# Optimization experiments

Measured on AMD Instinct MI355X. Metric: run time of the kernel, lower is better.

Reference implementation:

```python
import jax, jax.numpy as jnp
import numpy as np

N_NODES = 100000
N_EDGES = 1600000
IN_DIM, H1, H2, OUT_DIM = 128, 64, 32, 16


def setup_inputs() -> dict:
    key = jax.random.key(0)
    ks = jax.random.split(key, 9)
    x = jax.random.normal(ks[0], (N_NODES, IN_DIM), dtype=jnp.float32)
    edge_index = jax.random.randint(ks[1], (2, N_EDGES), 0, N_NODES, dtype=jnp.int64)
    # nn.Linear-style params (out_feats, in_feats) + bias
    def lin(k, o, i):
        bound = 1.0 / np.sqrt(i)
        kw, kb = jax.random.split(k)
        W = jax.random.uniform(kw, (o, i), jnp.float32, -bound, bound)
        b = jax.random.uniform(kb, (o,), jnp.float32, -bound, bound)
        return W, b
    W1, b1 = lin(ks[2], H1, IN_DIM)
    W2, b2 = lin(ks[3], H2, H1)
    Wf, bf = lin(ks[4], OUT_DIM, H2)
    return {"x": x, "edge_index": edge_index, "W1": W1, "b1": b1,
            "W2": W2, "b2": b2, "Wf": Wf, "bf": bf}


def reference(x, edge_index, W1, b1, W2, b2, Wf, bf):
    # Original: adj = to_dense_adj(edge_index); graph built from adj.T; DGL
    # copy_src+sum then gives new_h[src] = sum over dst of h[dst], i.e. A @ h
    # with A[src, dst]. No activation between layers (unused in forward),
    # dropout inactive at inference.
    N = x.shape[0]
    src, dst = edge_index[0], edge_index[1]

    def aggregate(h):  # sum of out-neighbor features: [N, d]
        return jax.ops.segment_sum(h[dst], src, num_segments=N)

    h = aggregate(x) @ W1.T + b1          # [N, 64]
    h = aggregate(h) @ W2.T + b2          # [N, 32]
    pooled = jnp.max(h, axis=0)           # [32] global max pool over nodes
    return pooled @ Wf.T + bf             # [16]
```

## Files before the change

### kernel.cpp

```cpp
#include <hip/hip_runtime.h>

#define N_NODES 100000
#define N_EDGES 1600000
#define IN_DIM 128
#define H1_DIM 64
#define H2_DIM 32
#define OUT_DIM 16

#define NPB 64
#define KB 1563
#define OFFW (KB + 1)
#define NCH 256
#define CH_E (N_EDGES / NCH)
#define CAP2 1536
#define NBIN1 64
#define NBIN2 (NCH - NBIN1)
#define NGB 782

typedef __attribute__((ext_vector_type(8))) short short8;
typedef __attribute__((ext_vector_type(4))) float f32x4;

__device__ inline unsigned short f2b(float v) {
    unsigned u = __float_as_uint(v);
    u += 0x7FFF + ((u >> 16) & 1);
    return (unsigned short)(u >> 16);
}
__device__ inline short f2bs(float v) { return (short)f2b(v); }
__device__ inline unsigned f32_to_key(float v) {
    unsigned u = __float_as_uint(v);
    return (v >= 0.f) ? (u | 0x80000000u) : ~u;
}
__device__ __forceinline__ void acc8(float* a, uint4 v) {
    a[0] += __uint_as_float(v.x << 16);
    a[1] += __uint_as_float(v.x & 0xFFFF0000u);
    a[2] += __uint_as_float(v.y << 16);
    a[3] += __uint_as_float(v.y & 0xFFFF0000u);
    a[4] += __uint_as_float(v.z << 16);
    a[5] += __uint_as_float(v.z & 0xFFFF0000u);
    a[6] += __uint_as_float(v.w << 16);
    a[7] += __uint_as_float(v.w & 0xFFFF0000u);
}

__device__ __forceinline__ void bin_chunk(const int* __restrict__ src,
                                          const int* __restrict__ dst,
                                          unsigned* __restrict__ off,
                                          unsigned* __restrict__ grec, int c) {
    __shared__ int hist[2048];
    __shared__ int part[512];
    __shared__ int cur[2048];
    int t = threadIdx.x;
    int e0 = c * CH_E;
    for (int i = t; i < 2048; i += 512) hist[i] = 0;
    __syncthreads();
    for (int e = t; e < CH_E; e += 512) atomicAdd(&hist[src[e0 + e] >> 6], 1);
    __syncthreads();
    int h0 = hist[4 * t], h1 = hist[4 * t + 1], h2 = hist[4 * t + 2], h3 = hist[4 * t + 3];
    int tot = h0 + h1 + h2 + h3;
    part[t] = tot;
    __syncthreads();
    for (int o = 1; o < 512; o <<= 1) {
        int a = (t >= o) ? part[t - o] : 0;
        __syncthreads();
        part[t] += a;
        __syncthreads();
    }
    int gb = part[t] - tot;
    int o0 = gb, o1 = gb + h0, o2 = o1 + h1, o3 = o2 + h2;
    int b4 = 4 * t;
    cur[b4] = o0; cur[b4 + 1] = o1; cur[b4 + 2] = o2; cur[b4 + 3] = o3;
    if (b4 + 0 < KB) off[(size_t)c * OFFW + b4 + 0] = o0;
    if (b4 + 1 < KB) off[(size_t)c * OFFW + b4 + 1] = o1;
    if (b4 + 2 < KB) off[(size_t)c * OFFW + b4 + 2] = o2;
    if (b4 + 3 < KB) off[(size_t)c * OFFW + b4 + 3] = o3;
    if (t == 0) off[(size_t)c * OFFW + KB] = CH_E;
    __syncthreads();
    for (int e = t; e < CH_E; e += 512) {
        int s = src[e0 + e];
        int d = dst[e0 + e];
        int p = atomicAdd(&cur[s >> 6], 1);
        grec[(size_t)e0 + p] = ((unsigned)(s & 63) << 17) | (unsigned)d;
    }
}

__global__ __launch_bounds__(512) void k1_kernel(const int* __restrict__ src,
                                                 const int* __restrict__ dst,
                                                 unsigned* __restrict__ off,
                                                 unsigned* __restrict__ grec,
                                                 const float* __restrict__ W1,
                                                 const float* __restrict__ b1,
                                                 const float* __restrict__ W2,
                                                 unsigned short* __restrict__ Wcb,
                                                 float* __restrict__ cvb) {
    if (blockIdx.x < NBIN1) {
        bin_chunk(src, dst, off, grec, blockIdx.x);
        return;
    }
    int t = threadIdx.x;
    for (int idx = t; idx < H2_DIM * IN_DIM; idx += 512) {
        int j = idx >> 7, f = idx & 127;
        float acc = 0.f;
        for (int k = 0; k < H1_DIM; ++k)
            acc += W2[j * H1_DIM + k] * W1[k * IN_DIM + f];
        Wcb[idx] = f2b(acc);
    }
    if (t < H2_DIM) {
        float s = 0.f;
        for (int k = 0; k < H1_DIM; ++k) s += W2[t * H1_DIM + k] * b1[k];
        cvb[t] = s;
    }
}

__global__ __launch_bounds__(512) void k2_kernel(const int* __restrict__ src,
                                                 const int* __restrict__ dst,
                                                 unsigned* __restrict__ off,
                                                 unsigned* __restrict__ grec,
                                                 const float* __restrict__ x,
                                                 const unsigned short* __restrict__ Wcb,
                                                 unsigned short* __restrict__ yb) {
    if (blockIdx.x < NBIN2) {
        bin_chunk(src, dst, off, grec, NBIN1 + blockIdx.x);
        return;
    }
    int gb = blockIdx.x - NBIN2;
    int t = threadIdx.x;
    int w = t >> 6, l = t & 63;
    int row = l & 15, kg = l >> 4;
    int base = gb * 128 + w * 16;
    int node = base + row;
    int nclamp = (node < N_NODES) ? node : (N_NODES - 1);
    const float* xp = x + (size_t)nclamp * IN_DIM + kg * 8;
    const unsigned short* b0p = Wcb + (size_t)row * IN_DIM + kg * 8;
    const unsigned short* b1p = Wcb + (size_t)(16 + row) * IN_DIM + kg * 8;
    f32x4 acc0 = {0.f, 0.f, 0.f, 0.f}, acc1 = {0.f, 0.f, 0.f, 0.f};
#pragma unroll
    for (int kk = 0; kk < 4; ++kk) {
        float4 xa = *(const float4*)(xp + kk * 32);
        float4 xb = *(const float4*)(xp + kk * 32 + 4);
        short8 a;
        a[0] = f2bs(xa.x); a[1] = f2bs(xa.y); a[2] = f2bs(xa.z); a[3] = f2bs(xa.w);
        a[4] = f2bs(xb.x); a[5] = f2bs(xb.y); a[6] = f2bs(xb.z); a[7] = f2bs(xb.w);
        short8 b0 = *(const short8*)(b0p + kk * 32);
        short8 b1 = *(const short8*)(b1p + kk * 32);
        acc0 = __builtin_amdgcn_mfma_f32_16x16x32_bf16(a, b0, acc0, 0, 0, 0);
        acc1 = __builtin_amdgcn_mfma_f32_16x16x32_bf16(a, b1, acc1, 0, 0, 0);
    }
#pragma unroll
    for (int r = 0; r < 4; ++r) {
        int n2 = base + kg * 4 + r;
        if (n2 < N_NODES) {
            yb[(size_t)n2 * H2_DIM + row]      = f2b(acc0[r]);
            yb[(size_t)n2 * H2_DIM + 16 + row] = f2b(acc1[r]);
        }
    }
}

__global__ __launch_bounds__(512) void agg1_kernel(const unsigned short* __restrict__ in,
                                                   const unsigned* __restrict__ off,
                                                   const unsigned* __restrict__ grec,
                                                   unsigned* __restrict__ grec2,
                                                   unsigned* __restrict__ noff,
                                                   unsigned short* __restrict__ z1b) {
    __shared__ int pos[NCH + 1], sst[NCH], len[NCH];
    __shared__ int shist[64], scur2[64];
    __shared__ int sscan[65];
    __shared__ unsigned rbuf[CAP2];
    __shared__ unsigned sbuf[CAP2];
    __shared__ int s_cnt;
    int t = threadIdx.x;
    int b = blockIdx.x;
    int gid = t >> 4;
    int L = t & 15;
    int chunk = L & 3, subset = L >> 2;

    if (t < NCH) {
        unsigned o0 = off[(size_t)t * OFFW + b];
        unsigned o1 = off[(size_t)t * OFFW + b + 1];
        sst[t] = (int)o0;
        len[t] = (int)(o1 - o0);
        pos[t] = (int)(o1 - o0);
    }
    __syncthreads();
    for (int o = 1; o < NCH; o <<= 1) {
        int a = (t < NCH && t >= o) ? pos[t - o] : 0;
        __syncthreads();
        if (t < NCH) pos[t] += a;
        __syncthreads();
    }
    if (t < NCH) pos[t] -= len[t];
    if (t == NCH - 1) {
        pos[NCH] = pos[t] + len[t];
        s_cnt = min(pos[t] + len[t], CAP2);
    }
    __syncthreads();
    int cnt = s_cnt;
    for (int i = t; i < cnt; i += 512) {
        int lo = 0, hi = NCH;
#pragma unroll
        for (int s = 0; s < 8; ++s) {
            int mid = (lo + hi) >> 1;
            if (pos[mid] <= i) lo = mid; else hi = mid;
        }
        rbuf[i] = grec[(size_t)lo * CH_E + sst[lo] + (i - pos[lo])];
    }
    if (t < 64) shist[t] = 0;
    __syncthreads();
    for (int i = t; i < cnt; i += 512) atomicAdd(&shist[rbuf[i] >> 17], 1);
    __syncthreads();
    if (t < 64) scur2[t] = shist[t];
    __syncthreads();
    for (int o = 1; o < 64; o <<= 1) {
        int a = (t < 64 && t >= o) ? scur2[t - o] : 0;
        __syncthreads();
        if (t < 64) scur2[t] += a;
        __syncthreads();
    }
    if (t < 64) sscan[t] = scur2[t] - shist[t];
    if (t == 63) sscan[64] = scur2[63];
    __syncthreads();
    if (t < 64) scur2[t] = sscan[t];
    __syncthreads();
    for (int i = t; i < cnt; i += 512) {
        unsigned r = rbuf[i];
        int p = atomicAdd(&scur2[r >> 17], 1);
        if (p < CAP2) sbuf[p] = r;
    }
    __syncthreads();
    for (int i = t; i < cnt; i += 512) grec2[(size_t)b * CAP2 + i] = sbuf[i];
    if (t < 65) noff[(size_t)b * 65 + t] = (unsigned)sscan[t];
    __syncthreads();

    for (int sl = gid; sl < NPB; sl += 32) {
        int r0 = sscan[sl], r1 = sscan[sl + 1];
        float a[8] = {0.f, 0.f, 0.f, 0.f, 0.f, 0.f, 0.f, 0.f};
        float aa[8] = {0.f, 0.f, 0.f, 0.f, 0.f, 0.f, 0.f, 0.f};
        for (int e = r0; e < r1; e += 8) {
            int eA = e + subset, eB = e + 4 + subset;
            if (eA < r1) {
                unsigned rc = sbuf[eA];
                uint4 v = *(const uint4*)(in + (size_t)(rc & 0x1FFFFu) * H2_DIM + chunk * 8);
                acc8(a, v);
            }
            if (eB < r1) {
                unsigned rc = sbuf[eB];
                uint4 v = *(const uint4*)(in + (size_t)(rc & 0x1FFFFu) * H2_DIM + chunk * 8);
                acc8(aa, v);
            }
        }
#pragma unroll
        for (int j = 0; j < 8; ++j) {
            float s = a[j] + aa[j];
            s += __shfl_xor(s, 4);
            s += __shfl_xor(s, 8);
            a[j] = s;
        }
        int node = b * NPB + sl;
        if (node < N_NODES && subset == 0) {
            uint4 o;
            o.x = (unsigned)f2b(a[0]) | ((unsigned)f2b(a[1]) << 16);
            o.y = (unsigned)f2b(a[2]) | ((unsigned)f2b(a[3]) << 16);
            o.z = (unsigned)f2b(a[4]) | ((unsigned)f2b(a[5]) << 16);
            o.w = (unsigned)f2b(a[6]) | ((unsigned)f2b(a[7]) << 16);
            *(uint4*)(z1b + (size_t)node * H2_DIM + chunk * 8) = o;
        }
    }
}

__global__ __launch_bounds__(1024) void agg2_kernel(const unsigned short* __restrict__ in,
                                                    const unsigned* __restrict__ grec2,
                                                    const unsigned* __restrict__ noff,
                                                    const float* __restrict__ cvb,
                                                    const float* __restrict__ b2,
                                                    unsigned* __restrict__ pk) {
    __shared__ float smq[64][4][8];
    int t = threadIdx.x;
    int b = blockIdx.x;
    int gid = t >> 4;
    int L = t & 15;
    int chunk = L & 3, subset = L >> 2;

    int r0 = (int)noff[(size_t)b * 65 + gid];
    int r1 = (int)noff[(size_t)b * 65 + gid + 1];
    const unsigned* rp = grec2 + (size_t)b * CAP2;

    float a[8] = {0.f, 0.f, 0.f, 0.f, 0.f, 0.f, 0.f, 0.f};
    float aa[8] = {0.f, 0.f, 0.f, 0.f, 0.f, 0.f, 0.f, 0.f};
    for (int e = r0; e < r1; e += 8) {
        int eA = e + subset, eB = e + 4 + subset;
        if (eA < r1) {
            unsigned rc = rp[eA];
            uint4 v = *(const uint4*)(in + (size_t)(rc & 0x1FFFFu) * H2_DIM + chunk * 8);
            acc8(a, v);
        }
        if (eB < r1) {
            unsigned rc = rp[eB];
            uint4 v = *(const uint4*)(in + (size_t)(rc & 0x1FFFFu) * H2_DIM + chunk * 8);
            acc8(aa, v);
        }
    }
#pragma unroll
    for (int j = 0; j < 8; ++j) {
        float s = a[j] + aa[j];
        s += __shfl_xor(s, 4);
        s += __shfl_xor(s, 8);
        a[j] = s;
    }

    int node = b * NPB + gid;
    float m[8];
    float dg = (float)(r1 - r0);
#pragma unroll
    for (int j = 0; j < 8; ++j) {
        float v = a[j] + dg * cvb[chunk * 8 + j] + b2[chunk * 8 + j];
        m[j] = (node < N_NODES) ? v : -3.402823466e+38f;
    }
    if (subset == 0) {
#pragma unroll
        for (int j = 0; j < 8; ++j) smq[gid][chunk][j] = m[j];
    }
    __syncthreads();
    if (t < 32) {
        int c = t >> 3, j = t & 7;
        float mm = smq[0][c][j];
#pragma unroll
        for (int k = 1; k < 64; ++k) mm = fmaxf(mm, smq[k][c][j]);
        atomicMax(&pk[t], f32_to_key(mm));
    }
}

__global__ void final_kernel(const unsigned* __restrict__ pk,
                             const float* __restrict__ Wf,
                             const float* __restrict__ bfv,
                             float* __restrict__ out) {
    __shared__ float pooled[H2_DIM];
    int t = threadIdx.x;
    if (t < H2_DIM) {
        unsigned k = pk[t];
        unsigned u = (k & 0x80000000u) ? (k & 0x7FFFFFFFu) : ~k;
        pooled[t] = __uint_as_float(u);
    }
    __syncthreads();
    if (t < OUT_DIM) {
        float acc = bfv[t];
        for (int j = 0; j < H2_DIM; ++j)
            acc += Wf[t * H2_DIM + j] * pooled[j];
        out[t] = acc;
    }
}

extern "C" void kernel_launch(void* const* d_in, const int* in_sizes, int n_in,
                              void* d_out, int out_size, void* d_ws, size_t ws_size,
                              hipStream_t stream) {
    const float* x  = (const float*)d_in[0];
    const int*   ei = (const int*)d_in[1];
    const float* W1 = (const float*)d_in[2];
    const float* b1 = (const float*)d_in[3];
    const float* W2 = (const float*)d_in[4];
    const float* b2 = (const float*)d_in[5];
    const float* Wf = (const float*)d_in[6];
    const float* bf = (const float*)d_in[7];
    float* out = (float*)d_out;

    const int* src = ei;
    const int* dst = ei + N_EDGES;

    unsigned short* yb  = (unsigned short*)d_ws;
    unsigned short* z1b = yb + (size_t)N_NODES * H2_DIM;
    unsigned short* Wcb = z1b + (size_t)N_NODES * H2_DIM;
    float* cvb      = (float*)(Wcb + H2_DIM * IN_DIM);
    unsigned* pk    = (unsigned*)(cvb + H2_DIM);
    unsigned* off   = pk + H2_DIM;
    unsigned* grec  = off + (size_t)NCH * OFFW;
    unsigned* grec2 = grec + N_EDGES;
    unsigned* noff  = grec2 + (size_t)KB * CAP2;

    hipMemsetAsync(pk, 0, H2_DIM * sizeof(unsigned), stream);

    k1_kernel<<<NBIN1 + 1, 512, 0, stream>>>(src, dst, off, grec, W1, b1, W2, Wcb, cvb);
    k2_kernel<<<NBIN2 + NGB, 512, 0, stream>>>(src, dst, off, grec, x, Wcb, yb);

    agg1_kernel<<<KB, 512, 0, stream>>>(yb, off, grec, grec2, noff, z1b);
    agg2_kernel<<<KB, 1024, 0, stream>>>(z1b, grec2, noff, cvb, b2, pk);

    final_kernel<<<1, 64, 0, stream>>>(pk, Wf, bf, out);
}
```

Before: 120.6 us.

## Merge setup kernels and double nodes per aggregation block

```diff
diff --git a/kernel.cpp b/kernel.cpp
--- a/kernel.cpp
+++ b/kernel.cpp
@@ -7,14 +7,12 @@
 #define H2_DIM 32
 #define OUT_DIM 16
 
-#define NPB 64
-#define KB 1563
+#define NPB 128
+#define KB 782
 #define OFFW (KB + 1)
 #define NCH 256
 #define CH_E (N_EDGES / NCH)
-#define CAP2 1536
-#define NBIN1 64
-#define NBIN2 (NCH - NBIN1)
+#define CAP2 3072
 #define NGB 782
 
 typedef __attribute__((ext_vector_type(8))) short short8;
@@ -45,17 +43,17 @@
                                           const int* __restrict__ dst,
                                           unsigned* __restrict__ off,
                                           unsigned* __restrict__ grec, int c) {
-    __shared__ int hist[2048];
+    __shared__ int hist[1024];
     __shared__ int part[512];
-    __shared__ int cur[2048];
+    __shared__ int cur[1024];
     int t = threadIdx.x;
     int e0 = c * CH_E;
-    for (int i = t; i < 2048; i += 512) hist[i] = 0;
-    __syncthreads();
-    for (int e = t; e < CH_E; e += 512) atomicAdd(&hist[src[e0 + e] >> 6], 1);
-    __syncthreads();
-    int h0 = hist[4 * t], h1 = hist[4 * t + 1], h2 = hist[4 * t + 2], h3 = hist[4 * t + 3];
-    int tot = h0 + h1 + h2 + h3;
+    hist[t] = 0; hist[t + 512] = 0;
+    __syncthreads();
+    for (int e = t; e < CH_E; e += 512) atomicAdd(&hist[src[e0 + e] >> 7], 1);
+    __syncthreads();
+    int h0 = hist[2 * t], h1 = hist[2 * t + 1];
+    int tot = h0 + h1;
     part[t] = tot;
     __syncthreads();
     for (int o = 1; o < 512; o <<= 1) {
@@ -65,72 +63,59 @@
         __syncthreads();
     }
     int gb = part[t] - tot;
-    int o0 = gb, o1 = gb + h0, o2 = o1 + h1, o3 = o2 + h2;
-    int b4 = 4 * t;
-    cur[b4] = o0; cur[b4 + 1] = o1; cur[b4 + 2] = o2; cur[b4 + 3] = o3;
-    if (b4 + 0 < KB) off[(size_t)c * OFFW + b4 + 0] = o0;
-    if (b4 + 1 < KB) off[(size_t)c * OFFW + b4 + 1] = o1;
-    if (b4 + 2 < KB) off[(size_t)c * OFFW + b4 + 2] = o2;
-    if (b4 + 3 < KB) off[(size_t)c * OFFW + b4 + 3] = o3;
+    int o0 = gb, o1 = gb + h0;
+    int b2i = 2 * t;
+    cur[b2i] = o0; cur[b2i + 1] = o1;
+    if (b2i + 0 < KB) off[(size_t)c * OFFW + b2i + 0] = o0;
+    if (b2i + 1 < KB) off[(size_t)c * OFFW + b2i + 1] = o1;
     if (t == 0) off[(size_t)c * OFFW + KB] = CH_E;
     __syncthreads();
     for (int e = t; e < CH_E; e += 512) {
         int s = src[e0 + e];
         int d = dst[e0 + e];
-        int p = atomicAdd(&cur[s >> 6], 1);
-        grec[(size_t)e0 + p] = ((unsigned)(s & 63) << 17) | (unsigned)d;
-    }
-}
-
-__global__ __launch_bounds__(512) void k1_kernel(const int* __restrict__ src,
+        int p = atomicAdd(&cur[s >> 7], 1);
+        grec[(size_t)e0 + p] = ((unsigned)(s & 127) << 17) | (unsigned)d;
+    }
+}
+
+__global__ __launch_bounds__(512) void ka_kernel(const int* __restrict__ src,
                                                  const int* __restrict__ dst,
                                                  unsigned* __restrict__ off,
                                                  unsigned* __restrict__ grec,
+                                                 const float* __restrict__ x,
                                                  const float* __restrict__ W1,
                                                  const float* __restrict__ b1,
                                                  const float* __restrict__ W2,
-                                                 unsigned short* __restrict__ Wcb,
+                                                 unsigned short* __restrict__ yb,
                                                  float* __restrict__ cvb) {
-    if (blockIdx.x < NBIN1) {
+    __shared__ unsigned short wl[H2_DIM * 136];
+    if (blockIdx.x < NCH) {
         bin_chunk(src, dst, off, grec, blockIdx.x);
         return;
     }
+    int gb = blockIdx.x - NCH;
     int t = threadIdx.x;
     for (int idx = t; idx < H2_DIM * IN_DIM; idx += 512) {
         int j = idx >> 7, f = idx & 127;
         float acc = 0.f;
         for (int k = 0; k < H1_DIM; ++k)
             acc += W2[j * H1_DIM + k] * W1[k * IN_DIM + f];
-        Wcb[idx] = f2b(acc);
-    }
-    if (t < H2_DIM) {
+        wl[j * 136 + f] = f2b(acc);
+    }
+    if (gb == 0 && t < H2_DIM) {
         float s = 0.f;
         for (int k = 0; k < H1_DIM; ++k) s += W2[t * H1_DIM + k] * b1[k];
         cvb[t] = s;
     }
-}
-
-__global__ __launch_bounds__(512) void k2_kernel(const int* __restrict__ src,
-                                                 const int* __restrict__ dst,
-                                                 unsigned* __restrict__ off,
-                                                 unsigned* __restrict__ grec,
-                                                 const float* __restrict__ x,
-                                                 const unsigned short* __restrict__ Wcb,
-                                                 unsigned short* __restrict__ yb) {
-    if (blockIdx.x < NBIN2) {
-        bin_chunk(src, dst, off, grec, NBIN1 + blockIdx.x);
-        return;
-    }
-    int gb = blockIdx.x - NBIN2;
-    int t = threadIdx.x;
+    __syncthreads();
     int w = t >> 6, l = t & 63;
     int row = l & 15, kg = l >> 4;
     int base = gb * 128 + w * 16;
     int node = base + row;
     int nclamp = (node < N_NODES) ? node : (N_NODES - 1);
     const float* xp = x + (size_t)nclamp * IN_DIM + kg * 8;
-    const unsigned short* b0p = Wcb + (size_t)row * IN_DIM + kg * 8;
-    const unsigned short* b1p = Wcb + (size_t)(16 + row) * IN_DIM + kg * 8;
+    const unsigned short* b0p = wl + row * 136 + kg * 8;
+    const unsigned short* b1p = wl + (16 + row) * 136 + kg * 8;
     f32x4 acc0 = {0.f, 0.f, 0.f, 0.f}, acc1 = {0.f, 0.f, 0.f, 0.f};
 #pragma unroll
     for (int kk = 0; kk < 4; ++kk) {
@@ -160,9 +145,9 @@
                                                    unsigned* __restrict__ grec2,
                                                    unsigned* __restrict__ noff,
                                                    unsigned short* __restrict__ z1b) {
-    __shared__ int pos[NCH + 1], sst[NCH], len[NCH];
-    __shared__ int shist[64], scur2[64];
-    __shared__ int sscan[65];
+    __shared__ int pos[NCH + 1], sst[NCH];
+    __shared__ int shist[NPB], scur2[NPB];
+    __shared__ int sscan[NPB + 1];
     __shared__ unsigned rbuf[CAP2];
     __shared__ unsigned sbuf[CAP2];
     __shared__ int s_cnt;
@@ -172,12 +157,13 @@
     int L = t & 15;
     int chunk = L & 3, subset = L >> 2;
 
+    int mylen = 0;
     if (t < NCH) {
         unsigned o0 = off[(size_t)t * OFFW + b];
         unsigned o1 = off[(size_t)t * OFFW + b + 1];
         sst[t] = (int)o0;
-        len[t] = (int)(o1 - o0);
-        pos[t] = (int)(o1 - o0);
+        mylen = (int)(o1 - o0);
+        pos[t] = mylen;
     }
     __syncthreads();
     for (int o = 1; o < NCH; o <<= 1) {
@@ -186,10 +172,10 @@
         if (t < NCH) pos[t] += a;
         __syncthreads();
     }
-    if (t < NCH) pos[t] -= len[t];
+    if (t < NCH) pos[t] -= mylen;
     if (t == NCH - 1) {
-        pos[NCH] = pos[t] + len[t];
-        s_cnt = min(pos[t] + len[t], CAP2);
+        pos[NCH] = pos[t] + mylen;
+        s_cnt = min(pos[t] + mylen, CAP2);
     }
     __syncthreads();
     int cnt = s_cnt;
@@ -202,22 +188,22 @@
         }
         rbuf[i] = grec[(size_t)lo * CH_E + sst[lo] + (i - pos[lo])];
     }
-    if (t < 64) shist[t] = 0;
+    if (t < NPB) shist[t] = 0;
     __syncthreads();
     for (int i = t; i < cnt; i += 512) atomicAdd(&shist[rbuf[i] >> 17], 1);
     __syncthreads();
-    if (t < 64) scur2[t] = shist[t];
-    __syncthreads();
-    for (int o = 1; o < 64; o <<= 1) {
-        int a = (t < 64 && t >= o) ? scur2[t - o] : 0;
-        __syncthreads();
-        if (t < 64) scur2[t] += a;
-        __syncthreads();
-    }
-    if (t < 64) sscan[t] = scur2[t] - shist[t];
-    if (t == 63) sscan[64] = scur2[63];
-    __syncthreads();
-    if (t < 64) scur2[t] = sscan[t];
+    if (t < NPB) scur2[t] = shist[t];
+    __syncthreads();
+    for (int o = 1; o < NPB; o <<= 1) {
+        int a = (t < NPB && t >= o) ? scur2[t - o] : 0;
+        __syncthreads();
+        if (t < NPB) scur2[t] += a;
+        __syncthreads();
+    }
+    if (t < NPB) sscan[t] = scur2[t] - shist[t];
+    if (t == NPB - 1) sscan[NPB] = scur2[t];
+    __syncthreads();
+    if (t < NPB) scur2[t] = sscan[t];
     __syncthreads();
     for (int i = t; i < cnt; i += 512) {
         unsigned r = rbuf[i];
@@ -226,7 +212,7 @@
     }
     __syncthreads();
     for (int i = t; i < cnt; i += 512) grec2[(size_t)b * CAP2 + i] = sbuf[i];
-    if (t < 65) noff[(size_t)b * 65 + t] = (unsigned)sscan[t];
+    if (t < NPB + 1) noff[(size_t)b * (NPB + 1) + t] = (unsigned)sscan[t];
     __syncthreads();
 
     for (int sl = gid; sl < NPB; sl += 32) {
@@ -278,40 +264,44 @@
     int L = t & 15;
     int chunk = L & 3, subset = L >> 2;
 
-    int r0 = (int)noff[(size_t)b * 65 + gid];
-    int r1 = (int)noff[(size_t)b * 65 + gid + 1];
     const unsigned* rp = grec2 + (size_t)b * CAP2;
-
-    float a[8] = {0.f, 0.f, 0.f, 0.f, 0.f, 0.f, 0.f, 0.f};
-    float aa[8] = {0.f, 0.f, 0.f, 0.f, 0.f, 0.f, 0.f, 0.f};
-    for (int e = r0; e < r1; e += 8) {
-        int eA = e + subset, eB = e + 4 + subset;
-        if (eA < r1) {
-            unsigned rc = rp[eA];
-            uint4 v = *(const uint4*)(in + (size_t)(rc & 0x1FFFFu) * H2_DIM + chunk * 8);
-            acc8(a, v);
-        }
-        if (eB < r1) {
-            unsigned rc = rp[eB];
-            uint4 v = *(const uint4*)(in + (size_t)(rc & 0x1FFFFu) * H2_DIM + chunk * 8);
-            acc8(aa, v);
-        }
-    }
-#pragma unroll
-    for (int j = 0; j < 8; ++j) {
-        float s = a[j] + aa[j];
-        s += __shfl_xor(s, 4);
-        s += __shfl_xor(s, 8);
-        a[j] = s;
-    }
-
-    int node = b * NPB + gid;
+    const unsigned* np = noff + (size_t)b * (NPB + 1);
+
     float m[8];
-    float dg = (float)(r1 - r0);
-#pragma unroll
-    for (int j = 0; j < 8; ++j) {
-        float v = a[j] + dg * cvb[chunk * 8 + j] + b2[chunk * 8 + j];
-        m[j] = (node < N_NODES) ? v : -3.402823466e+38f;
+#pragma unroll
+    for (int j = 0; j < 8; ++j) m[j] = -3.402823466e+38f;
+
+    for (int sl = gid; sl < NPB; sl += 64) {
+        int r0 = (int)np[sl], r1 = (int)np[sl + 1];
+        float a[8] = {0.f, 0.f, 0.f, 0.f, 0.f, 0.f, 0.f, 0.f};
+        float aa[8] = {0.f, 0.f, 0.f, 0.f, 0.f, 0.f, 0.f, 0.f};
+        for (int e = r0; e < r1; e += 8) {
+            int eA = e + subset, eB = e + 4 + subset;
+            if (eA < r1) {
+                unsigned rc = rp[eA];
+                uint4 v = *(const uint4*)(in + (size_t)(rc & 0x1FFFFu) * H2_DIM + chunk * 8);
+                acc8(a, v);
+            }
+            if (eB < r1) {
+                unsigned rc = rp[eB];
+                uint4 v = *(const uint4*)(in + (size_t)(rc & 0x1FFFFu) * H2_DIM + chunk * 8);
+                acc8(aa, v);
+            }
+        }
+#pragma unroll
+        for (int j = 0; j < 8; ++j) {
+            float s = a[j] + aa[j];
+            s += __shfl_xor(s, 4);
+            s += __shfl_xor(s, 8);
+            a[j] = s;
+        }
+        int node = b * NPB + sl;
+        if (node < N_NODES) {
+            float dg = (float)(r1 - r0);
+#pragma unroll
+            for (int j = 0; j < 8; ++j)
+                m[j] = fmaxf(m[j], a[j] + dg * cvb[chunk * 8 + j] + b2[chunk * 8 + j]);
+        }
     }
     if (subset == 0) {
 #pragma unroll
@@ -365,8 +355,7 @@
 
     unsigned short* yb  = (unsigned short*)d_ws;
     unsigned short* z1b = yb + (size_t)N_NODES * H2_DIM;
-    unsigned short* Wcb = z1b + (size_t)N_NODES * H2_DIM;
-    float* cvb      = (float*)(Wcb + H2_DIM * IN_DIM);
+    float* cvb      = (float*)(z1b + (size_t)N_NODES * H2_DIM);
     unsigned* pk    = (unsigned*)(cvb + H2_DIM);
     unsigned* off   = pk + H2_DIM;
     unsigned* grec  = off + (size_t)NCH * OFFW;
@@ -375,8 +364,7 @@
 
     hipMemsetAsync(pk, 0, H2_DIM * sizeof(unsigned), stream);
 
-    k1_kernel<<<NBIN1 + 1, 512, 0, stream>>>(src, dst, off, grec, W1, b1, W2, Wcb, cvb);
-    k2_kernel<<<NBIN2 + NGB, 512, 0, stream>>>(src, dst, off, grec, x, Wcb, yb);
+    ka_kernel<<<NCH + NGB, 512, 0, stream>>>(src, dst, off, grec, x, W1, b1, W2, yb, cvb);
 
     agg1_kernel<<<KB, 512, 0, stream>>>(yb, off, grec, grec2, noff, z1b);
     agg2_kernel<<<KB, 1024, 0, stream>>>(z1b, grec2, noff, cvb, b2, pk);
```

Measured after the change: 143.8 us. 19.3% more time.
